# Kernel tuning notes

Hardware: AMD Instinct MI355X
Metric: run time of the kernel (lower is better)

The kernel has to match this reference:

```python
import jax, jax.numpy as jnp
import numpy as np

N = 20000
E = 320000
CIN = 16
COUT = 16
D = 4
RADIUS = 0.5


def setup_inputs() -> dict:
    key = jax.random.key(0)
    k1, k2, k3, k4 = jax.random.split(key, 4)
    positions = jax.random.uniform(k1, (N, 3), dtype=jnp.float32)
    features = jax.random.normal(k2, (N, CIN), dtype=jnp.float32)
    filters = jax.random.normal(k3, (D, D, D, CIN, COUT), dtype=jnp.float32)
    edge_index = jax.random.randint(k4, (2, E), 0, N, dtype=jnp.int32)
    return {"positions": positions, "features": features,
            "filters": filters, "edge_index": edge_index}


def _trilinear(filters, gc):
    # Replicates torch grid_sample(align_corners=True) semantics used by the
    # module: grid coord (x,y,z) indexes spatial dims (W,H,D), i.e. gc[:,0]
    # samples filter axis 2, gc[:,1] axis 1, gc[:,2] axis 0.
    Dres = filters.shape[0]
    a, b, c = gc[:, 2], gc[:, 1], gc[:, 0]  # axes 0, 1, 2 of filters
    a0f, b0f, c0f = jnp.floor(a), jnp.floor(b), jnp.floor(c)
    a0 = jnp.clip(a0f.astype(jnp.int32), 0, Dres - 1)
    b0 = jnp.clip(b0f.astype(jnp.int32), 0, Dres - 1)
    c0 = jnp.clip(c0f.astype(jnp.int32), 0, Dres - 1)
    a1 = jnp.minimum(a0 + 1, Dres - 1)
    b1 = jnp.minimum(b0 + 1, Dres - 1)
    c1 = jnp.minimum(c0 + 1, Dres - 1)
    ad = (a - a0f)[:, None, None]  # (E,1,1)
    bd = (b - b0f)[:, None, None]
    cd = (c - c0f)[:, None, None]

    g = lambda i, j, k: filters[i, j, k]  # (E, CIN, COUT) gather
    f00 = g(a0, b0, c0) * (1 - cd) + g(a0, b0, c1) * cd
    f01 = g(a0, b1, c0) * (1 - cd) + g(a0, b1, c1) * cd
    f10 = g(a1, b0, c0) * (1 - cd) + g(a1, b0, c1) * cd
    f11 = g(a1, b1, c0) * (1 - cd) + g(a1, b1, c1) * cd
    f0 = f00 * (1 - bd) + f01 * bd
    f1 = f10 * (1 - bd) + f11 * bd
    return f0 * (1 - ad) + f1 * ad  # (E, CIN, COUT)


def reference(positions, features, filters, edge_index):
    row, col = edge_index[0], edge_index[1]
    r = positions[col] - positions[row]                  # (E,3)
    dist2 = jnp.sum(r * r, axis=-1)                      # (E,)
    valid = (dist2 < RADIUS ** 2).astype(positions.dtype)
    window = (1.0 - dist2 / RADIUS ** 2) ** 3 * valid
    norm = jnp.sqrt(dist2)[:, None]
    mapped = r / (norm + 1e-8) * jnp.tanh(norm)          # ball -> cube, (E,3)
    gc = (mapped + 1.0) * ((filters.shape[0] - 1) / 2.0) # (E,3) in [0, D-1]
    filt = _trilinear(filters, gc)                       # (E, CIN, COUT)
    conv_edge = jnp.einsum('eio,ei->eo', filt, features[col])
    conv_edge = conv_edge * window[:, None]
    n_nodes = positions.shape[0]
    sums = jax.ops.segment_sum(conv_edge, row, num_segments=n_nodes)
    cnt = jax.ops.segment_sum(jnp.ones((conv_edge.shape[0],), positions.dtype),
                              row, num_segments=n_nodes)
    return sums / jnp.maximum(cnt, 1.0)[:, None]         # scatter-mean
```

## Files before the change

kernel.cpp:

```cpp
#include <hip/hip_runtime.h>
#include <hip/hip_fp16.h>
#include <math.h>

#define NN 20000
#define EE 320000
#define CIN 16
#define COUT 16
#define R2C 0.25f
#define MAXDEG 64
#define SLOTC_OFF 81920
#define P_OFF     163840
#define CONV_OFF  (163840 + 40960000)

__global__ __launch_bounds__(256) void k_zero(float* __restrict__ out, int* __restrict__ cnt) {
    int i = blockIdx.x * 256 + threadIdx.x;
    if (i < NN * COUT) out[i] = 0.0f;
    if (i < NN) cnt[i] = 0;
}

__global__ __launch_bounds__(256) void k_pgemm(const float* __restrict__ feat,
                                               const float* __restrict__ filt,
                                               __half* __restrict__ P,
                                               int* __restrict__ cnt_all,
                                               int* __restrict__ slotc) {
    __shared__ float fl[16 * 256];

    if (blockIdx.y == 0) {
        int g = blockIdx.x * 256 + threadIdx.x;
        if (g < NN) { cnt_all[g] = 0; slotc[g] = 0; }
    }

    {
        const float4* src = (const float4*)(filt + (size_t)blockIdx.y * 16 * 256);
        float4* dst = (float4*)fl;
        #pragma unroll
        for (int r = 0; r < 4; ++r)
            dst[r * 256 + threadIdx.x] = src[r * 256 + threadIdx.x];
    }
    __syncthreads();

    int lane  = threadIdx.x & 63;
    int w     = threadIdx.x >> 6;
    int q     = lane & 3;
    int ns    = lane >> 2;
    int nbase = blockIdx.x * 64;

    float f[4][16];
    #pragma unroll
    for (int r = 0; r < 4; ++r) {
        int n = nbase + ns + 16 * r;
        if (n < NN) {
            const float4* fp = (const float4*)(feat + (size_t)n * 16);
            float4 f0 = fp[0], f1 = fp[1], f2 = fp[2], f3 = fp[3];
            f[r][0]=f0.x; f[r][1]=f0.y; f[r][2]=f0.z; f[r][3]=f0.w;
            f[r][4]=f1.x; f[r][5]=f1.y; f[r][6]=f1.z; f[r][7]=f1.w;
            f[r][8]=f2.x; f[r][9]=f2.y; f[r][10]=f2.z; f[r][11]=f2.w;
            f[r][12]=f3.x; f[r][13]=f3.y; f[r][14]=f3.z; f[r][15]=f3.w;
        } else {
            #pragma unroll
            for (int ci = 0; ci < 16; ++ci) f[r][ci] = 0.0f;
        }
    }

    #pragma unroll
    for (int c = 0; c < 4; ++c) {
        int cell = w * 4 + c;
        float4 acc0 = make_float4(0.f,0.f,0.f,0.f);
        float4 acc1 = acc0, acc2 = acc0, acc3 = acc0;
        const float4* row = (const float4*)(fl + cell * 256) + q;
        #pragma unroll
        for (int ci = 0; ci < 16; ++ci) {
            float4 wv = row[ci * 4];
            float v0 = f[0][ci], v1 = f[1][ci], v2 = f[2][ci], v3 = f[3][ci];
            acc0.x = fmaf(v0, wv.x, acc0.x); acc0.y = fmaf(v0, wv.y, acc0.y);
            acc0.z = fmaf(v0, wv.z, acc0.z); acc0.w = fmaf(v0, wv.w, acc0.w);
            acc1.x = fmaf(v1, wv.x, acc1.x); acc1.y = fmaf(v1, wv.y, acc1.y);
            acc1.z = fmaf(v1, wv.z, acc1.z); acc1.w = fmaf(v1, wv.w, acc1.w);
            acc2.x = fmaf(v2, wv.x, acc2.x); acc2.y = fmaf(v2, wv.y, acc2.y);
            acc2.z = fmaf(v2, wv.z, acc2.z); acc2.w = fmaf(v2, wv.w, acc2.w);
            acc3.x = fmaf(v3, wv.x, acc3.x); acc3.y = fmaf(v3, wv.y, acc3.y);
            acc3.z = fmaf(v3, wv.z, acc3.z); acc3.w = fmaf(v3, wv.w, acc3.w);
        }
        size_t cell_g = (size_t)(blockIdx.y * 16 + cell);
        float4 accs[4] = {acc0, acc1, acc2, acc3};
        #pragma unroll
        for (int r = 0; r < 4; ++r) {
            int n = nbase + ns + 16 * r;
            if (n < NN) {
                __half2 lo = __float22half2_rn(make_float2(accs[r].x, accs[r].y));
                __half2 hi = __float22half2_rn(make_float2(accs[r].z, accs[r].w));
                uint2 u;
                u.x = *(unsigned int*)&lo;
                u.y = *(unsigned int*)&hi;
                *(uint2*)(P + (cell_g * NN + n) * 16 + q * 4) = u;
            }
        }
    }
}

__device__ __forceinline__ bool edge_geom(const float* __restrict__ pos, int row, int col,
                                          float& win,
                                          int ia[2], int jb[2], int kc[2],
                                          float wa[2], float wb[2], float wc[2]) {
    float rx = pos[col*3+0] - pos[row*3+0];
    float ry = pos[col*3+1] - pos[row*3+1];
    float rz = pos[col*3+2] - pos[row*3+2];
    float d2 = rx*rx + ry*ry + rz*rz;
    if (!(d2 < R2C)) return false;
    float u = 1.0f - d2 / R2C;
    win = u * u * u;
    float nr = sqrtf(d2);
    float s  = tanhf(nr) / (nr + 1e-8f);
    float gx = (rx * s + 1.0f) * 1.5f;
    float gy = (ry * s + 1.0f) * 1.5f;
    float gz = (rz * s + 1.0f) * 1.5f;
    float af = floorf(gz), bf = floorf(gy), cf = floorf(gx);
    int ia0 = min(max((int)af, 0), 3);
    int ib0 = min(max((int)bf, 0), 3);
    int ic0 = min(max((int)cf, 0), 3);
    ia[0] = ia0; ia[1] = min(ia0 + 1, 3);
    jb[0] = ib0; jb[1] = min(ib0 + 1, 3);
    kc[0] = ic0; kc[1] = min(ic0 + 1, 3);
    float ad = gz - af, bd = gy - bf, cd = gx - cf;
    wa[0] = 1.0f - ad; wa[1] = ad;
    wb[0] = 1.0f - bd; wb[1] = bd;
    wc[0] = 1.0f - cd; wc[1] = cd;
    return true;
}

__global__ __launch_bounds__(256) void k_edge_store(const float* __restrict__ pos,
                                                    const int* __restrict__ ei,
                                                    const __half* __restrict__ P,
                                                    __half* __restrict__ conv,
                                                    int* __restrict__ cnt_all,
                                                    int* __restrict__ slotc) {
    long long t = (long long)blockIdx.x * 256 + threadIdx.x;
    int e = (int)(t >> 3);
    int h = (int)(t & 7);
    if (e >= EE) return;
    int row = ei[e];
    int col = ei[EE + e];
    int lane = threadIdx.x & 63;

    if (h == 0) atomicAdd(&cnt_all[row], 1);

    float win;
    int ia[2], jb[2], kc[2];
    float wa[2], wb[2], wc[2];
    bool valid = edge_geom(pos, row, col, win, ia, jb, kc, wa, wb, wc);

    if (valid) {
        int sv = 0;
        if (h == 0) sv = atomicAdd(&slotc[row], 1);
        int slot = __shfl(sv, lane & 56, 64);

        float2 acc = make_float2(0.f, 0.f);
        const __half* Pq = P + (size_t)col * 16 + h * 2;
        #pragma unroll
        for (int da = 0; da < 2; ++da)
        #pragma unroll
        for (int db = 0; db < 2; ++db)
        #pragma unroll
        for (int dc = 0; dc < 2; ++dc) {
            float w = wa[da] * wb[db] * wc[dc] * win;
            int cell = ia[da]*16 + jb[db]*4 + kc[dc];
            unsigned int raw = *(const unsigned int*)(Pq + (size_t)cell * NN * 16);
            __half2 hv = *(__half2*)&raw;
            float2 p = __half22float2(hv);
            acc.x = fmaf(w, p.x, acc.x);
            acc.y = fmaf(w, p.y, acc.y);
        }
        if (slot < MAXDEG) {
            __half2 hv = __float22half2_rn(acc);
            *(__half2*)(conv + ((size_t)row * MAXDEG + slot) * 16 + h * 2) = hv;
        }
    }
}

__global__ __launch_bounds__(256) void k_gather(const __half* __restrict__ conv,
                                                const int* __restrict__ cnt_all,
                                                const int* __restrict__ slotc,
                                                float* __restrict__ out) {
    int t = blockIdx.x * 256 + threadIdx.x;
    int n = t >> 3;
    int h = t & 7;
    if (n >= NN) return;
    int deg = min(slotc[n], MAXDEG);
    int ca  = cnt_all[n];
    float2 acc = make_float2(0.f, 0.f);
    const __half* base = conv + (size_t)n * MAXDEG * 16 + h * 2;
    for (int s = 0; s < deg; ++s) {
        __half2 hv = *(const __half2*)(base + (size_t)s * 16);
        float2 p = __half22float2(hv);
        acc.x += p.x;
        acc.y += p.y;
    }
    float inv = 1.0f / (float)max(ca, 1);
    float2 r = make_float2(acc.x * inv, acc.y * inv);
    *(float2*)(out + (size_t)n * 16 + h * 2) = r;
}

__global__ __launch_bounds__(256) void k_edge_direct(const float* __restrict__ pos,
                                                     const float* __restrict__ feat,
                                                     const float* __restrict__ filt,
                                                     const int* __restrict__ ei,
                                                     float* __restrict__ out,
                                                     int* __restrict__ cnt) {
    int e = blockIdx.x * 256 + threadIdx.x;
    if (e >= EE) return;
    int row = ei[e];
    int col = ei[EE + e];
    atomicAdd(&cnt[row], 1);

    float win;
    int ia[2], jb[2], kc[2];
    float wa[2], wb[2], wc[2];
    if (!edge_geom(pos, row, col, win, ia, jb, kc, wa, wb, wc)) return;

    float fv[16];
    const float4* fp = (const float4*)(feat + (size_t)col * 16);
    float4 f0 = fp[0], f1 = fp[1], f2 = fp[2], f3 = fp[3];
    fv[0]=f0.x; fv[1]=f0.y; fv[2]=f0.z; fv[3]=f0.w;
    fv[4]=f1.x; fv[5]=f1.y; fv[6]=f1.z; fv[7]=f1.w;
    fv[8]=f2.x; fv[9]=f2.y; fv[10]=f2.z; fv[11]=f2.w;
    fv[12]=f3.x; fv[13]=f3.y; fv[14]=f3.z; fv[15]=f3.w;

    float4 a0 = make_float4(0.f,0.f,0.f,0.f);
    float4 a1 = a0, a2 = a0, a3 = a0;
    for (int da = 0; da < 2; ++da)
    for (int db = 0; db < 2; ++db)
    for (int dc = 0; dc < 2; ++dc) {
        float w = wa[da] * wb[db] * wc[dc] * win;
        const float* fb = filt + (size_t)(ia[da]*16 + jb[db]*4 + kc[dc]) * 256;
        #pragma unroll
        for (int ci = 0; ci < 16; ++ci) {
            float c = w * fv[ci];
            const float4* r4 = (const float4*)(fb + ci * 16);
            float4 w0 = r4[0], w1 = r4[1], w2 = r4[2], w3 = r4[3];
            a0.x = fmaf(c, w0.x, a0.x); a0.y = fmaf(c, w0.y, a0.y);
            a0.z = fmaf(c, w0.z, a0.z); a0.w = fmaf(c, w0.w, a0.w);
            a1.x = fmaf(c, w1.x, a1.x); a1.y = fmaf(c, w1.y, a1.y);
            a1.z = fmaf(c, w1.z, a1.z); a1.w = fmaf(c, w1.w, a1.w);
            a2.x = fmaf(c, w2.x, a2.x); a2.y = fmaf(c, w2.y, a2.y);
            a2.z = fmaf(c, w2.z, a2.z); a2.w = fmaf(c, w2.w, a2.w);
            a3.x = fmaf(c, w3.x, a3.x); a3.y = fmaf(c, w3.y, a3.y);
            a3.z = fmaf(c, w3.z, a3.z); a3.w = fmaf(c, w3.w, a3.w);
        }
    }
    float* op = out + (size_t)row * 16;
    atomicAdd(op+0,  a0.x); atomicAdd(op+1,  a0.y); atomicAdd(op+2,  a0.z); atomicAdd(op+3,  a0.w);
    atomicAdd(op+4,  a1.x); atomicAdd(op+5,  a1.y); atomicAdd(op+6,  a1.z); atomicAdd(op+7,  a1.w);
    atomicAdd(op+8,  a2.x); atomicAdd(op+9,  a2.y); atomicAdd(op+10, a2.z); atomicAdd(op+11, a2.w);
    atomicAdd(op+12, a3.x); atomicAdd(op+13, a3.y); atomicAdd(op+14, a3.z); atomicAdd(op+15, a3.w);
}

__global__ __launch_bounds__(256) void k_div(float* __restrict__ out, const int* __restrict__ cnt) {
    int i = blockIdx.x * 256 + threadIdx.x;
    if (i >= NN * COUT) return;
    int c = cnt[i >> 4];
    float denom = (c > 1) ? (float)c : 1.0f;
    out[i] = out[i] / denom;
}

extern "C" void kernel_launch(void* const* d_in, const int* in_sizes, int n_in,
                              void* d_out, int out_size, void* d_ws, size_t ws_size,
                              hipStream_t stream) {
    const float* pos  = (const float*)d_in[0];
    const float* feat = (const float*)d_in[1];
    const float* filt = (const float*)d_in[2];
    const int*   ei   = (const int*)d_in[3];
    float* out = (float*)d_out;

    int*    cnt_all = (int*)d_ws;
    int*    slotc   = (int*)((char*)d_ws + SLOTC_OFF);
    __half* P       = (__half*)((char*)d_ws + P_OFF);
    __half* conv    = (__half*)((char*)d_ws + CONV_OFF);

    size_t need = (size_t)CONV_OFF + (size_t)NN * MAXDEG * 16 * sizeof(__half);

    if (ws_size >= need) {
        dim3 pg((NN + 63) / 64, 4);
        k_pgemm<<<pg, 256, 0, stream>>>(feat, filt, P, cnt_all, slotc);
        long long tot = (long long)EE * 8;
        k_edge_store<<<(int)((tot + 255) / 256), 256, 0, stream>>>(pos, ei, P, conv, cnt_all, slotc);
        k_gather<<<(NN * 8 + 255) / 256, 256, 0, stream>>>(conv, cnt_all, slotc, out);
    } else {
        k_zero<<<(NN * COUT + 255) / 256, 256, 0, stream>>>(out, cnt_all);
        k_edge_direct<<<(EE + 255) / 256, 256, 0, stream>>>(pos, feat, filt, ei, out, cnt_all);
        k_div<<<(NN * COUT + 255) / 256, 256, 0, stream>>>(out, cnt_all);
    }
}
```

Measured before the change: 108.0 us.

## Replace per-cell feature-filter precompute with per-edge fp16 dot products from LDS filters

Drops the precomputed P table (64 cells × N × 16 in fp16, about 40 MB), which each edge gathered from 8 corners. Instead, each edge compacts the valid edges in its wavefront with a ballot and loads the fp16 filter bank into LDS. Every lane then computes one output channel as 8 corner dot products using fdot2 on fp16 features and filters. Global traffic shrinks, at the cost of more per-edge ALU work and LDS reads. The conv buffer is now fp32, and corner-index clamping is changed to 0..2.

```diff
diff --git a/kernel.cpp b/kernel.cpp
--- a/kernel.cpp
+++ b/kernel.cpp
@@ -8,94 +8,212 @@
 #define COUT 16
 #define R2C 0.25f
 #define MAXDEG 64
+
 #define SLOTC_OFF 81920
-#define P_OFF     163840
-#define CONV_OFF  (163840 + 40960000)
+#define FILTH_OFF 163840
+#define FEATH_OFF 196608
+#define CONV_OFF  836608
+
+typedef _Float16 h2 __attribute__((ext_vector_type(2)));
+
+#if defined(__has_builtin)
+# if __has_builtin(__builtin_amdgcn_fdot2)
+#  define HAS_FDOT2 1
+# endif
+#endif
+#ifndef HAS_FDOT2
+# define HAS_FDOT2 0
+#endif
+
+__device__ __forceinline__ h2 as_h2(unsigned int x) {
+    union { unsigned int u; h2 h; } v; v.u = x; return v.h;
+}
+
+__global__ __launch_bounds__(256) void k_prep(const float* __restrict__ feat,
+                                              const float* __restrict__ filt,
+                                              __half* __restrict__ featH,
+                                              __half* __restrict__ filtH,
+                                              int* __restrict__ cnt_all,
+                                              int* __restrict__ slotc) {
+    int t = blockIdx.x * 256 + threadIdx.x;
+    if (t < NN) { cnt_all[t] = 0; slotc[t] = 0; }
+    if (t < 16384) {
+        int cell = t >> 8, rem = t & 255, ci = rem >> 4, oo = rem & 15;
+        int d = cell * 256 + (ci >> 3) * 128 + oo * 8 + (ci & 7);
+        filtH[d] = __float2half(filt[t]);
+    }
+    if (t < NN * 16) featH[t] = __float2half(feat[t]);
+}
+
+__global__ __launch_bounds__(256) void k_edge(const float* __restrict__ pos,
+                                              const int* __restrict__ ei,
+                                              const __half* __restrict__ featH,
+                                              const uint4* __restrict__ filtH4,
+                                              float* __restrict__ conv,
+                                              int* __restrict__ cnt_all,
+                                              int* __restrict__ slotc) {
+    __shared__ uint4 sf[2048];
+    #pragma unroll
+    for (int r = 0; r < 8; ++r)
+        sf[r * 256 + threadIdx.x] = filtH4[r * 256 + threadIdx.x];
+    __syncthreads();
+
+    int lane = threadIdx.x & 63;
+    int gid  = lane >> 4;
+    int o    = lane & 15;
+    int e = (blockIdx.x * 4 + (threadIdx.x >> 6)) * 64 + lane;
+
+    int row = ei[e];
+    int col = ei[EE + e];
+    atomicAdd(&cnt_all[row], 1);
+
+    float rx = pos[col*3+0] - pos[row*3+0];
+    float ry = pos[col*3+1] - pos[row*3+1];
+    float rz = pos[col*3+2] - pos[row*3+2];
+    float d2 = rx*rx + ry*ry + rz*rz;
+    bool valid = d2 < R2C;
+
+    float win = 0.f, ad = 0.f, bd = 0.f, cd = 0.f;
+    int colidx = 0, rowslot = 0;
+    if (valid) {
+        float u = 1.0f - d2 * 4.0f;
+        win = u * u * u;
+        float nr = sqrtf(d2);
+        float s  = tanhf(nr) / (nr + 1e-8f);
+        float gx = (rx * s + 1.0f) * 1.5f;
+        float gy = (ry * s + 1.0f) * 1.5f;
+        float gz = (rz * s + 1.0f) * 1.5f;
+        float af = floorf(gz), bf = floorf(gy), cf = floorf(gx);
+        int ia0 = min(max((int)af, 0), 2);
+        int jb0 = min(max((int)bf, 0), 2);
+        int kc0 = min(max((int)cf, 0), 2);
+        ad = gz - af; bd = gy - bf; cd = gx - cf;
+        colidx = col | (ia0 << 20) | (jb0 << 24) | (kc0 << 28);
+        int slot = atomicAdd(&slotc[row], 1);
+        rowslot = row | (min(slot, MAXDEG) << 16);
+    }
+
+    unsigned long long bal = __ballot(valid);
+    int nv = __popcll(bal);
+    unsigned long long m0 = bal;
+    unsigned long long m1 = m0 & (m0 - 1);
+    unsigned long long m2 = m1 & (m1 - 1);
+    unsigned long long m3 = m2 & (m2 - 1);
+
+    for (int k = 0; k < nv; k += 4) {
+        unsigned long long mg = (gid == 0) ? m0 : (gid == 1) ? m1 : (gid == 2) ? m2 : m3;
+        bool active = (k + gid) < nv;
+        int src = active ? (int)__builtin_ctzll(mg) : 0;
+
+        float win_s = __shfl(win, src, 64);
+        float ad_s  = __shfl(ad,  src, 64);
+        float bd_s  = __shfl(bd,  src, 64);
+        float cd_s  = __shfl(cd,  src, 64);
+        int   ci_s  = __shfl(colidx,  src, 64);
+        int   rs_s  = __shfl(rowslot, src, 64);
+
+        m0 = m3 & (m3 - 1);
+        m1 = m0 & (m0 - 1);
+        m2 = m1 & (m1 - 1);
+        m3 = m2 & (m2 - 1);
+
+        if (active) {
+            int col_s  = ci_s & 0xFFFFF;
+            int ia0 = (ci_s >> 20) & 3, jb0 = (ci_s >> 24) & 3, kc0 = (ci_s >> 28) & 3;
+            int row_s  = rs_s & 0xFFFF;
+            int slot_s = rs_s >> 16;
+
+            const uint4* fb = (const uint4*)(featH + (size_t)col_s * 16);
+            uint4 fA = fb[0], fB = fb[1];
+
+            float va0 = (1.f - ad_s) * win_s, va1 = ad_s * win_s;
+            float vb0 = 1.f - bd_s, vb1 = bd_s;
+            float vc0 = 1.f - cd_s, vc1 = cd_s;
+            float p00 = va0*vb0, p01 = va0*vb1, p10 = va1*vb0, p11 = va1*vb1;
+            float w8[8] = { p00*vc0, p00*vc1, p01*vc0, p01*vc1,
+                            p10*vc0, p10*vc1, p11*vc0, p11*vc1 };
+
+            int bi = ((ia0 * 16 + jb0 * 4 + kc0) << 5) + o;
+            const int cofs[8] = {0, 32, 128, 160, 512, 544, 640, 672};
+
+            float acc = 0.f;
+#if HAS_FDOT2
+            h2 ft0 = as_h2(fA.x), ft1 = as_h2(fA.y), ft2 = as_h2(fA.z), ft3 = as_h2(fA.w);
+            h2 ft4 = as_h2(fB.x), ft5 = as_h2(fB.y), ft6 = as_h2(fB.z), ft7 = as_h2(fB.w);
+            #pragma unroll
+            for (int c = 0; c < 8; ++c) {
+                uint4 g0 = sf[bi + cofs[c]];
+                uint4 g1 = sf[bi + cofs[c] + 16];
+                float d = 0.f;
+                d = __builtin_amdgcn_fdot2(as_h2(g0.x), ft0, d, false);
+                d = __builtin_amdgcn_fdot2(as_h2(g0.y), ft1, d, false);
+                d = __builtin_amdgcn_fdot2(as_h2(g0.z), ft2, d, false);
+                d = __builtin_amdgcn_fdot2(as_h2(g0.w), ft3, d, false);
+                d = __builtin_amdgcn_fdot2(as_h2(g1.x), ft4, d, false);
+                d = __builtin_amdgcn_fdot2(as_h2(g1.y), ft5, d, false);
+                d = __builtin_amdgcn_fdot2(as_h2(g1.z), ft6, d, false);
+                d = __builtin_amdgcn_fdot2(as_h2(g1.w), ft7, d, false);
+                acc = fmaf(w8[c], d, acc);
+            }
+#else
+            float ftf[16];
+            { h2 t;
+              t = as_h2(fA.x); ftf[0]=(float)t.x;  ftf[1]=(float)t.y;
+              t = as_h2(fA.y); ftf[2]=(float)t.x;  ftf[3]=(float)t.y;
+              t = as_h2(fA.z); ftf[4]=(float)t.x;  ftf[5]=(float)t.y;
+              t = as_h2(fA.w); ftf[6]=(float)t.x;  ftf[7]=(float)t.y;
+              t = as_h2(fB.x); ftf[8]=(float)t.x;  ftf[9]=(float)t.y;
+              t = as_h2(fB.y); ftf[10]=(float)t.x; ftf[11]=(float)t.y;
+              t = as_h2(fB.z); ftf[12]=(float)t.x; ftf[13]=(float)t.y;
+              t = as_h2(fB.w); ftf[14]=(float)t.x; ftf[15]=(float)t.y; }
+            #pragma unroll
+            for (int c = 0; c < 8; ++c) {
+                uint4 g0 = sf[bi + cofs[c]];
+                uint4 g1 = sf[bi + cofs[c] + 16];
+                float d = 0.f;
+                h2 t;
+                t = as_h2(g0.x); d = fmaf((float)t.x, ftf[0],  d); d = fmaf((float)t.y, ftf[1],  d);
+                t = as_h2(g0.y); d = fmaf((float)t.x, ftf[2],  d); d = fmaf((float)t.y, ftf[3],  d);
+                t = as_h2(g0.z); d = fmaf((float)t.x, ftf[4],  d); d = fmaf((float)t.y, ftf[5],  d);
+                t = as_h2(g0.w); d = fmaf((float)t.x, ftf[6],  d); d = fmaf((float)t.y, ftf[7],  d);
+                t = as_h2(g1.x); d = fmaf((float)t.x, ftf[8],  d); d = fmaf((float)t.y, ftf[9],  d);
+                t = as_h2(g1.y); d = fmaf((float)t.x, ftf[10], d); d = fmaf((float)t.y, ftf[11], d);
+                t = as_h2(g1.z); d = fmaf((float)t.x, ftf[12], d); d = fmaf((float)t.y, ftf[13], d);
+                t = as_h2(g1.w); d = fmaf((float)t.x, ftf[14], d); d = fmaf((float)t.y, ftf[15], d);
+                acc = fmaf(w8[c], d, acc);
+            }
+#endif
+            if (slot_s < MAXDEG)
+                conv[((size_t)row_s * MAXDEG + slot_s) * 16 + o] = acc;
+        }
+    }
+}
+
+__global__ __launch_bounds__(256) void k_gather(const float* __restrict__ conv,
+                                                const int* __restrict__ cnt_all,
+                                                const int* __restrict__ slotc,
+                                                float* __restrict__ out) {
+    int t = blockIdx.x * 256 + threadIdx.x;
+    int n = t >> 3;
+    int h = t & 7;
+    if (n >= NN) return;
+    int deg = min(slotc[n], MAXDEG);
+    int ca  = cnt_all[n];
+    float2 acc = make_float2(0.f, 0.f);
+    const float2* base = (const float2*)(conv + (size_t)n * MAXDEG * 16) + h;
+    for (int s = 0; s < deg; ++s) {
+        float2 p = base[(size_t)s * 8];
+        acc.x += p.x;
+        acc.y += p.y;
+    }
+    float inv = 1.0f / (float)max(ca, 1);
+    *(float2*)(out + (size_t)n * 16 + h * 2) = make_float2(acc.x * inv, acc.y * inv);
+}
 
 __global__ __launch_bounds__(256) void k_zero(float* __restrict__ out, int* __restrict__ cnt) {
     int i = blockIdx.x * 256 + threadIdx.x;
     if (i < NN * COUT) out[i] = 0.0f;
     if (i < NN) cnt[i] = 0;
-}
-
-__global__ __launch_bounds__(256) void k_pgemm(const float* __restrict__ feat,
-                                               const float* __restrict__ filt,
-                                               __half* __restrict__ P,
-                                               int* __restrict__ cnt_all,
-                                               int* __restrict__ slotc) {
-    __shared__ float fl[16 * 256];
-
-    if (blockIdx.y == 0) {
-        int g = blockIdx.x * 256 + threadIdx.x;
-        if (g < NN) { cnt_all[g] = 0; slotc[g] = 0; }
-    }
-
-    {
-        const float4* src = (const float4*)(filt + (size_t)blockIdx.y * 16 * 256);
-        float4* dst = (float4*)fl;
-        #pragma unroll
-        for (int r = 0; r < 4; ++r)
-            dst[r * 256 + threadIdx.x] = src[r * 256 + threadIdx.x];
-    }
-    __syncthreads();
-
-    int lane  = threadIdx.x & 63;
-    int w     = threadIdx.x >> 6;
-    int q     = lane & 3;
-    int ns    = lane >> 2;
-    int nbase = blockIdx.x * 64;
-
-    float f[4][16];
-    #pragma unroll
-    for (int r = 0; r < 4; ++r) {
-        int n = nbase + ns + 16 * r;
-        if (n < NN) {
-            const float4* fp = (const float4*)(feat + (size_t)n * 16);
-            float4 f0 = fp[0], f1 = fp[1], f2 = fp[2], f3 = fp[3];
-            f[r][0]=f0.x; f[r][1]=f0.y; f[r][2]=f0.z; f[r][3]=f0.w;
-            f[r][4]=f1.x; f[r][5]=f1.y; f[r][6]=f1.z; f[r][7]=f1.w;
-            f[r][8]=f2.x; f[r][9]=f2.y; f[r][10]=f2.z; f[r][11]=f2.w;
-            f[r][12]=f3.x; f[r][13]=f3.y; f[r][14]=f3.z; f[r][15]=f3.w;
-        } else {
-            #pragma unroll
-            for (int ci = 0; ci < 16; ++ci) f[r][ci] = 0.0f;
-        }
-    }
-
-    #pragma unroll
-    for (int c = 0; c < 4; ++c) {
-        int cell = w * 4 + c;
-        float4 acc0 = make_float4(0.f,0.f,0.f,0.f);
-        float4 acc1 = acc0, acc2 = acc0, acc3 = acc0;
-        const float4* row = (const float4*)(fl + cell * 256) + q;
-        #pragma unroll
-        for (int ci = 0; ci < 16; ++ci) {
-            float4 wv = row[ci * 4];
-            float v0 = f[0][ci], v1 = f[1][ci], v2 = f[2][ci], v3 = f[3][ci];
-            acc0.x = fmaf(v0, wv.x, acc0.x); acc0.y = fmaf(v0, wv.y, acc0.y);
-            acc0.z = fmaf(v0, wv.z, acc0.z); acc0.w = fmaf(v0, wv.w, acc0.w);
-            acc1.x = fmaf(v1, wv.x, acc1.x); acc1.y = fmaf(v1, wv.y, acc1.y);
-            acc1.z = fmaf(v1, wv.z, acc1.z); acc1.w = fmaf(v1, wv.w, acc1.w);
-            acc2.x = fmaf(v2, wv.x, acc2.x); acc2.y = fmaf(v2, wv.y, acc2.y);
-            acc2.z = fmaf(v2, wv.z, acc2.z); acc2.w = fmaf(v2, wv.w, acc2.w);
-            acc3.x = fmaf(v3, wv.x, acc3.x); acc3.y = fmaf(v3, wv.y, acc3.y);
-            acc3.z = fmaf(v3, wv.z, acc3.z); acc3.w = fmaf(v3, wv.w, acc3.w);
-        }
-        size_t cell_g = (size_t)(blockIdx.y * 16 + cell);
-        float4 accs[4] = {acc0, acc1, acc2, acc3};
-        #pragma unroll
-        for (int r = 0; r < 4; ++r) {
-            int n = nbase + ns + 16 * r;
-            if (n < NN) {
-                __half2 lo = __float22half2_rn(make_float2(accs[r].x, accs[r].y));
-                __half2 hi = __float22half2_rn(make_float2(accs[r].z, accs[r].w));
-                uint2 u;
-                u.x = *(unsigned int*)&lo;
-                u.y = *(unsigned int*)&hi;
-                *(uint2*)(P + (cell_g * NN + n) * 16 + q * 4) = u;
-            }
-        }
-    }
 }
 
 __device__ __forceinline__ bool edge_geom(const float* __restrict__ pos, int row, int col,
@@ -128,78 +246,6 @@
     return true;
 }
 
-__global__ __launch_bounds__(256) void k_edge_store(const float* __restrict__ pos,
-                                                    const int* __restrict__ ei,
-                                                    const __half* __restrict__ P,
-                                                    __half* __restrict__ conv,
-                                                    int* __restrict__ cnt_all,
-                                                    int* __restrict__ slotc) {
-    long long t = (long long)blockIdx.x * 256 + threadIdx.x;
-    int e = (int)(t >> 3);
-    int h = (int)(t & 7);
-    if (e >= EE) return;
-    int row = ei[e];
-    int col = ei[EE + e];
-    int lane = threadIdx.x & 63;
-
-    if (h == 0) atomicAdd(&cnt_all[row], 1);
-
-    float win;
-    int ia[2], jb[2], kc[2];
-    float wa[2], wb[2], wc[2];
-    bool valid = edge_geom(pos, row, col, win, ia, jb, kc, wa, wb, wc);
-
-    if (valid) {
-        int sv = 0;
-        if (h == 0) sv = atomicAdd(&slotc[row], 1);
-        int slot = __shfl(sv, lane & 56, 64);
-
-        float2 acc = make_float2(0.f, 0.f);
-        const __half* Pq = P + (size_t)col * 16 + h * 2;
-        #pragma unroll
-        for (int da = 0; da < 2; ++da)
-        #pragma unroll
-        for (int db = 0; db < 2; ++db)
-        #pragma unroll
-        for (int dc = 0; dc < 2; ++dc) {
-            float w = wa[da] * wb[db] * wc[dc] * win;
-            int cell = ia[da]*16 + jb[db]*4 + kc[dc];
-            unsigned int raw = *(const unsigned int*)(Pq + (size_t)cell * NN * 16);
-            __half2 hv = *(__half2*)&raw;
-            float2 p = __half22float2(hv);
-            acc.x = fmaf(w, p.x, acc.x);
-            acc.y = fmaf(w, p.y, acc.y);
-        }
-        if (slot < MAXDEG) {
-            __half2 hv = __float22half2_rn(acc);
-            *(__half2*)(conv + ((size_t)row * MAXDEG + slot) * 16 + h * 2) = hv;
-        }
-    }
-}
-
-__global__ __launch_bounds__(256) void k_gather(const __half* __restrict__ conv,
-                                                const int* __restrict__ cnt_all,
-                                                const int* __restrict__ slotc,
-                                                float* __restrict__ out) {
-    int t = blockIdx.x * 256 + threadIdx.x;
-    int n = t >> 3;
-    int h = t & 7;
-    if (n >= NN) return;
-    int deg = min(slotc[n], MAXDEG);
-    int ca  = cnt_all[n];
-    float2 acc = make_float2(0.f, 0.f);
-    const __half* base = conv + (size_t)n * MAXDEG * 16 + h * 2;
-    for (int s = 0; s < deg; ++s) {
-        __half2 hv = *(const __half2*)(base + (size_t)s * 16);
-        float2 p = __half22float2(hv);
-        acc.x += p.x;
-        acc.y += p.y;
-    }
-    float inv = 1.0f / (float)max(ca, 1);
-    float2 r = make_float2(acc.x * inv, acc.y * inv);
-    *(float2*)(out + (size_t)n * 16 + h * 2) = r;
-}
-
 __global__ __launch_bounds__(256) void k_edge_direct(const float* __restrict__ pos,
                                                      const float* __restrict__ feat,
                                                      const float* __restrict__ filt,
@@ -273,16 +319,15 @@
 
     int*    cnt_all = (int*)d_ws;
     int*    slotc   = (int*)((char*)d_ws + SLOTC_OFF);
-    __half* P       = (__half*)((char*)d_ws + P_OFF);
-    __half* conv    = (__half*)((char*)d_ws + CONV_OFF);
-
-    size_t need = (size_t)CONV_OFF + (size_t)NN * MAXDEG * 16 * sizeof(__half);
+    __half* filtH   = (__half*)((char*)d_ws + FILTH_OFF);
+    __half* featH   = (__half*)((char*)d_ws + FEATH_OFF);
+    float*  conv    = (float*)((char*)d_ws + CONV_OFF);
+
+    size_t need = (size_t)CONV_OFF + (size_t)NN * MAXDEG * 16 * sizeof(float);
 
     if (ws_size >= need) {
-        dim3 pg((NN + 63) / 64, 4);
-        k_pgemm<<<pg, 256, 0, stream>>>(feat, filt, P, cnt_all, slotc);
-        long long tot = (long long)EE * 8;
-        k_edge_store<<<(int)((tot + 255) / 256), 256, 0, stream>>>(pos, ei, P, conv, cnt_all, slotc);
+        k_prep<<<1250, 256, 0, stream>>>(feat, filt, featH, filtH, cnt_all, slotc);
+        k_edge<<<1250, 256, 0, stream>>>(pos, ei, featH, (const uint4*)filtH, conv, cnt_all, slotc);
         k_gather<<<(NN * 8 + 255) / 256, 256, 0, stream>>>(conv, cnt_all, slotc, out);
     } else {
         k_zero<<<(NN * COUT + 255) / 256, 256, 0, stream>>>(out, cnt_all);
```

Result: faster. 96.77 us (-10.4%).
